# Optimization experiments

Measured on AMD Instinct MI355X. Metric: run time of the kernel, lower is better.

## Reference

```python
import jax, jax.numpy as jnp
import numpy as np

N, T, H, L, E, F, CN, CG = 20000, 2, 128, 4, 320000, 514, 3, 2
EPS = 1e-7  # GENConv message epsilon


def _ln(x, g, b):
    mu = jnp.mean(x, axis=-1, keepdims=True)
    var = jnp.mean((x - mu) ** 2, axis=-1, keepdims=True)
    return (x - mu) / jnp.sqrt(var + 1e-5) * g + b


def _genconv(x, src, dst, e, W1, b1, g1, be1, W2, b2, t, n):
    # message: relu(x_j + edge_attr) + eps
    msg = jax.nn.relu(x[src] + e) + EPS  # [E,H]
    # softmax aggregation with learnable temperature t, grouped by dst
    logits = msg * t
    m = jax.ops.segment_max(logits, dst, num_segments=n)
    m = jnp.where(jnp.isfinite(m), m, 0.0)  # guard empty segments
    ex = jnp.exp(logits - m[dst])
    denom = jax.ops.segment_sum(ex, dst, num_segments=n)
    alpha = ex / (denom[dst] + 1e-16)
    agg = jax.ops.segment_sum(msg * alpha, dst, num_segments=n)  # [N,H]
    out = agg + x  # residual with root node (x_r)
    # MLP: Lin(H,2H) -> LayerNorm -> ReLU -> Lin(2H,H)
    h1 = jax.nn.relu(_ln(out @ W1 + b1, g1, be1))
    return h1 @ W2 + b2


def _attn(x, Wq, Wk, Wv, gamma):
    # x: [N, T, H]; channel (transform-axis) self-attention, gamma-gated residual
    q = jnp.einsum('tc,nch->nth', Wq, x)
    k = jnp.einsum('tc,nch->nth', Wk, x)
    v = jnp.einsum('tc,nch->nth', Wv, x)
    a = jax.nn.softmax(jnp.einsum('nth,nsh->nts', q, k), axis=-1)
    o = jnp.einsum('nts,nsh->nth', a, v)
    return gamma * o + x


def setup_inputs() -> dict:
    key = jax.random.key(0)
    ks = iter(jax.random.split(key, 48))

    def nrm(sh, s=0.02):
        return jax.random.normal(next(ks), sh, dtype=jnp.float32) * s

    inp = {}
    inp['node_feature'] = jax.random.normal(next(ks), (N, F), dtype=jnp.float32)
    inp['edge_index'] = jax.random.randint(next(ks), (T, 2, E), 0, N, dtype=jnp.int32)
    inp['edge_attr'] = jax.random.normal(next(ks), (T, E, 2), dtype=jnp.float32)
    # encoders
    inp['Wne'] = nrm((F, H)); inp['bne'] = jnp.zeros((H,), jnp.float32)
    inp['Wee'] = nrm((2, H)); inp['bee'] = jnp.zeros((H,), jnp.float32)
    # per-layer GENConv MLP params (stacked over L)
    inp['W1'] = nrm((L, H, 2 * H)); inp['b1'] = jnp.zeros((L, 2 * H), jnp.float32)
    inp['g1'] = jnp.ones((L, 2 * H), jnp.float32); inp['be1'] = jnp.zeros((L, 2 * H), jnp.float32)
    inp['W2'] = nrm((L, 2 * H, H)); inp['b2'] = jnp.zeros((L, H), jnp.float32)
    # DeepGCNLayer LayerNorms
    inp['dg'] = jnp.ones((L, H), jnp.float32); inp['db'] = jnp.zeros((L, H), jnp.float32)
    # learnable temperatures
    inp['t'] = jnp.ones((L,), jnp.float32)
    # node attention + head
    inp['Wq_n'] = nrm((T, T), 0.2); inp['Wk_n'] = nrm((T, T), 0.2); inp['Wv_n'] = nrm((T, T), 0.2)
    inp['gamma_n'] = jnp.float32(0.5)
    inp['Wn1'] = nrm((T * H, T * H)); inp['bn1'] = jnp.zeros((T * H,), jnp.float32)
    inp['Wn2'] = nrm((T * H, CN)); inp['bn2'] = jnp.zeros((CN,), jnp.float32)
    # graph attention + head
    inp['Wq_g'] = nrm((T, T), 0.2); inp['Wk_g'] = nrm((T, T), 0.2); inp['Wv_g'] = nrm((T, T), 0.2)
    inp['gamma_g'] = jnp.float32(0.5)
    inp['Wg1'] = nrm((T * H, T * H)); inp['bg1'] = jnp.zeros((T * H,), jnp.float32)
    inp['Wg2'] = nrm((T * H, CG)); inp['bg2'] = jnp.zeros((CG,), jnp.float32)
    return inp


def reference(node_feature, edge_index, edge_attr, Wne, bne, Wee, bee,
              W1, b1, g1, be1, W2, b2, dg, db, t,
              Wq_n, Wk_n, Wv_n, gamma_n, Wn1, bn1, Wn2, bn2,
              Wq_g, Wk_g, Wv_g, gamma_g, Wg1, bg1, Wg2, bg2):
    embs = []
    for ti in range(T):
        x = node_feature @ Wne + bne           # node_encoder
        e = edge_attr[ti] @ Wee + bee          # edge_encoder
        src, dst = edge_index[ti, 0], edge_index[ti, 1]
        # layers[0].conv applied directly
        x = _genconv(x, src, dst, e, W1[0], b1[0], g1[0], be1[0], W2[0], b2[0], t[0], N)
        # res+ DeepGCN blocks
        for l in range(1, L):
            h = jax.nn.relu(_ln(x, dg[l], db[l]))  # dropout p=0.1 is identity in eval
            x = x + _genconv(h, src, dst, e, W1[l], b1[l], g1[l], be1[l], W2[l], b2[l], t[l], N)
        x = jax.nn.relu(_ln(x, dg[0], db[0]))
        embs.append(x)
    emb = jnp.stack(embs, axis=1)  # [N, T, H]

    a = _attn(emb, Wq_n, Wk_n, Wv_n, gamma_n).reshape(N, T * H)
    node = jax.nn.relu(a @ Wn1 + bn1) @ Wn2 + bn2
    node = jax.nn.log_softmax(node, axis=-1)

    g = _attn(emb, Wq_g, Wk_g, Wv_g, gamma_g).reshape(N, T * H)
    gp = jnp.mean(g, axis=0, keepdims=True)  # global_mean_pool (single graph)
    gp = jax.nn.relu(gp @ Wg1 + bg1) @ Wg2 + bg2
    gp = jax.nn.log_softmax(gp, axis=-1)
    return (node, gp)
```

## Files before the change

kernel.cpp:

```cpp
#include <hip/hip_runtime.h>

#define NN 20000
#define TT 2
#define HH 128
#define LL 4
#define EE 320000
#define FF 514
#define CN 3
#define CG 2
#define MP 20096

typedef __bf16 bf16x8 __attribute__((ext_vector_type(8)));
typedef __bf16 bf16x4 __attribute__((ext_vector_type(4)));
typedef __bf16 bf16x2 __attribute__((ext_vector_type(2)));
typedef float f32x4 __attribute__((ext_vector_type(4)));

struct __align__(8) Edge { int src; __bf16 ea0, ea1; };

__device__ inline float wave_sum(float v) {
#pragma unroll
  for (int off = 32; off; off >>= 1) v += __shfl_xor(v, off);
  return v;
}
__device__ inline float red16(float v) {
  v += __shfl_xor(v, 1); v += __shfl_xor(v, 2);
  v += __shfl_xor(v, 4); v += __shfl_xor(v, 8);
  return v;
}

__device__ __forceinline__ float fexp2(float x) {
#if __has_builtin(__builtin_amdgcn_exp2f)
  return __builtin_amdgcn_exp2f(x);
#else
  return exp2f(x);
#endif
}

__device__ __forceinline__ void gload_lds16(const void* g, void* l) {
  __builtin_amdgcn_global_load_lds(
      (const __attribute__((address_space(1))) unsigned int*)g,
      (__attribute__((address_space(3))) unsigned int*)l, 16, 0, 0);
}

#define ENCB (MP / 64)
#define SSB 313
#define CHUNK 5000
__global__ __launch_bounds__(256) void enc_scatter_kernel(
    const float* __restrict__ Af, const __bf16* __restrict__ BT,
    const float* __restrict__ bias, __bf16* __restrict__ C,
    const int* __restrict__ edge_index, const float* __restrict__ edge_attr,
    int* __restrict__ cursor, Edge* __restrict__ edges) {
  __shared__ __bf16 As[2][64][32];
  __shared__ __bf16 Bs[2][128][32];
  const int tid = threadIdx.x;
  if (blockIdx.x >= ENCB) {
    int sb = blockIdx.x - ENCB;
    int chunk = sb & 7;
    int slice = sb >> 3;
    int i0 = slice * 2048 + tid * 8;
    if (i0 >= 2 * EE) return;
    int ti = (i0 >= EE) ? 1 : 0;
    int e0 = i0 - ti * EE;
    const int* srcp = edge_index + (size_t)ti * 2 * EE;
    int dst8[8];
    __builtin_memcpy(dst8, srcp + EE + e0, 32);
#pragma unroll
    for (int j = 0; j < 8; ++j) {
      int gnode = ti * NN + dst8[j];
      if (gnode / CHUNK != chunk) continue;
      int s = srcp[e0 + j];
      float2 ea = ((const float2*)edge_attr)[(size_t)ti * EE + e0 + j];
      int pos = atomicAdd(&cursor[gnode], 1);
      Edge ed;
      ed.src = s + ti * MP;
      ed.ea0 = (__bf16)ea.x; ed.ea1 = (__bf16)ea.y;
      __builtin_memcpy(&edges[pos], &ed, sizeof(Edge));
    }
    return;
  }
  const int K = 576;
  const int lane = tid & 63, w = tid >> 6;
  const int bm = blockIdx.x * 64;
  const int wr = (w >> 1) * 32, wc = (w & 1) * 64;
  const int fr = lane & 15, fq = lane >> 4;
  const int rowA = tid >> 2, chA = (tid & 3) * 8;
  const bool rowOK = (bm + rowA) < NN;
  const float* Arow = Af + (size_t)(bm + rowA) * FF;
  const __bf16* Bb = BT + (size_t)rowA * K + chA;
  const __bf16* Bb2 = Bb + (size_t)64 * K;
  f32x4 acc[2][4] = {};
  float va[8];

#define LOADA(k0)                                                   \
  do {                                                              \
    int c0_ = (k0) + chA;                                           \
    if (rowOK && c0_ + 8 <= FF) {                                   \
      __builtin_memcpy(va, Arow + c0_, 32);                         \
    } else {                                                        \
      _Pragma("unroll") for (int i_ = 0; i_ < 8; ++i_)              \
          va[i_] = (rowOK && c0_ + i_ < FF) ? Arow[c0_ + i_] : 0.f; \
    }                                                               \
  } while (0)
#define WRITEA(buf)                                                 \
  do {                                                              \
    bf16x8 o_;                                                      \
    _Pragma("unroll") for (int i_ = 0; i_ < 8; ++i_)                \
        o_[i_] = (__bf16)va[i_];                                    \
    *(bf16x8*)&As[buf][rowA][chA] = o_;                             \
  } while (0)
#define STAGEB(buf, k0)                                 \
  do {                                                  \
    gload_lds16(Bb + (k0), &Bs[buf][rowA][chA]);        \
    gload_lds16(Bb2 + (k0), &Bs[buf][rowA + 64][chA]);  \
  } while (0)

  LOADA(0); WRITEA(0);
  STAGEB(0, 0);
  __syncthreads();
  int cur = 0;
  for (int k0 = 0; k0 < K; k0 += 32) {
    bool last = (k0 + 32 >= K);
    if (!last) {
      LOADA(k0 + 32);
      STAGEB(cur ^ 1, k0 + 32);
    }
    bf16x8 af[2], bq[4];
#pragma unroll
    for (int m = 0; m < 2; ++m)
      af[m] = *(const bf16x8*)&As[cur][wr + m * 16 + fr][fq * 8];
#pragma unroll
    for (int n = 0; n < 4; ++n)
      bq[n] = *(const bf16x8*)&Bs[cur][wc + n * 16 + fr][fq * 8];
#pragma unroll
    for (int m = 0; m < 2; ++m)
#pragma unroll
      for (int n = 0; n < 4; ++n)
        acc[m][n] =
            __builtin_amdgcn_mfma_f32_16x16x32_bf16(af[m], bq[n], acc[m][n], 0, 0, 0);
    if (!last) WRITEA(cur ^ 1);
    __syncthreads();
    cur ^= 1;
  }
#undef LOADA
#undef WRITEA
#undef STAGEB
#pragma unroll
  for (int m = 0; m < 2; ++m) {
#pragma unroll
    for (int n = 0; n < 4; ++n) {
#pragma unroll
      for (int j = 0; j < 4; ++j) {
        int gm = bm + wr + m * 16 + fq * 4 + j;
        int gn = wc + n * 16 + fr;
        if (gm < NN) {
          __bf16 c = (__bf16)(acc[m][n][j] + bias[gn]);
          C[(size_t)gm * 128 + gn] = c;
          C[(size_t)(gm + MP) * 128 + gn] = c;
        }
      }
    }
  }
}

__global__ __launch_bounds__(256) void gemm256_head(
    const __bf16* __restrict__ A, const __bf16* __restrict__ BT,
    const float* __restrict__ bias, const float* __restrict__ W2h,
    const float* __restrict__ b2h, float* __restrict__ outf, int M, int K) {
  __shared__ __bf16 As[2][64][32];
  __shared__ __bf16 Bs[2][256][32];
  const int tid = threadIdx.x;
  const int lane = tid & 63, w = tid >> 6;
  const int bm = blockIdx.x * 64;
  const int wr = w * 16;
  const int fr = lane & 15, fq = lane >> 4;
  const int rowA = tid >> 2, chA = (tid & 3) * 8;
  const __bf16* Ab = A + (size_t)(bm + rowA) * K + chA;
  const __bf16* Bb = BT + (size_t)rowA * K + chA;
  f32x4 acc[16] = {};

#define STG(buf, k0)                                                \
  do {                                                              \
    gload_lds16(Ab + (k0), &As[buf][rowA][chA]);                    \
    _Pragma("unroll") for (int r = 0; r < 4; ++r)                   \
        gload_lds16(Bb + (size_t)(r * 64) * K + (k0),               \
                    &Bs[buf][rowA + r * 64][chA]);                  \
  } while (0)

  STG(0, 0);
  __syncthreads();
  int cur = 0;
  for (int k0 = 0; k0 < K; k0 += 32) {
    if (k0 + 32 < K) STG(cur ^ 1, k0 + 32);
    bf16x8 af = *(const bf16x8*)&As[cur][wr + fr][fq * 8];
#pragma unroll
    for (int n = 0; n < 16; ++n) {
      bf16x8 bq = *(const bf16x8*)&Bs[cur][n * 16 + fr][fq * 8];
      acc[n] = __builtin_amdgcn_mfma_f32_16x16x32_bf16(af, bq, acc[n], 0, 0, 0);
    }
    __syncthreads();
    cur ^= 1;
  }
#undef STG

  float cb[16], w0[16], w1[16], w2[16];
#pragma unroll
  for (int n = 0; n < 16; ++n) {
    int col = n * 16 + fr;
    cb[n] = bias[col];
    w0[n] = W2h[col * 3 + 0];
    w1[n] = W2h[col * 3 + 1];
    w2[n] = W2h[col * 3 + 2];
  }
#pragma unroll
  for (int j = 0; j < 4; ++j) {
    float p0 = 0.f, p1 = 0.f, p2 = 0.f;
#pragma unroll
    for (int n = 0; n < 16; ++n) {
      float h = fmaxf(acc[n][j] + cb[n], 0.f);
      p0 += h * w0[n]; p1 += h * w1[n]; p2 += h * w2[n];
    }
    p0 = red16(p0); p1 = red16(p1); p2 = red16(p2);
    int gm = bm + wr + fq * 4 + j;
    if (fr == 0 && gm < M) {
      float l0 = p0 + b2h[0], l1 = p1 + b2h[1], l2 = p2 + b2h[2];
      float m = fmaxf(l0, fmaxf(l1, l2));
      float lse = m + logf(__expf(l0 - m) + __expf(l1 - m) + __expf(l2 - m));
      outf[(size_t)gm * 3 + 0] = l0 - lse;
      outf[(size_t)gm * 3 + 1] = l1 - lse;
      outf[(size_t)gm * 3 + 2] = l2 - lse;
    }
  }
}

template <int MODE>
__global__ __launch_bounds__(256) void gemm_layer(
    const __bf16* __restrict__ A, const __bf16* __restrict__ W1T,
    const float* __restrict__ b1, const float* __restrict__ g1,
    const float* __restrict__ be1, const __bf16* __restrict__ W2T,
    const float* __restrict__ b2, float* __restrict__ xres,
    const float* __restrict__ dgv, const float* __restrict__ dbv,
    void* __restrict__ lnout) {
  __shared__ char smem[40960];
  __shared__ __bf16 h1[64][264];
  __shared__ float redS[64][2], redS2[64][2];
  auto As = (__bf16(*)[64][32])smem;
  auto Bs1 = (__bf16(*)[256][32])(smem + 8192);
  auto Bs2 = (__bf16(*)[128][32])smem;
  const int tid = threadIdx.x;
  const int lane = tid & 63, w = tid >> 6;
  const int bm = blockIdx.x * 64;
  const int fr = lane & 15, fq = lane >> 4;
  const int rowA = tid >> 2, chA = (tid & 3) * 8;

  {
    const int wr = w * 16;
    const __bf16* Ab = A + (size_t)(bm + rowA) * 128 + chA;
    const __bf16* Bb = W1T + (size_t)rowA * 128 + chA;
    f32x4 acc[16] = {};
#define STG1(buf, k0)                                                 \
  do {                                                                \
    gload_lds16(Ab + (k0), &As[buf][rowA][chA]);                      \
    _Pragma("unroll") for (int r = 0; r < 4; ++r)                     \
        gload_lds16(Bb + (size_t)(r * 64) * 128 + (k0),               \
                    &Bs1[buf][rowA + r * 64][chA]);                   \
  } while (0)
    STG1(0, 0);
    __syncthreads();
    int cur = 0;
    for (int k0 = 0; k0 < 128; k0 += 32) {
      if (k0 + 32 < 128) STG1(cur ^ 1, k0 + 32);
      bf16x8 af = *(const bf16x8*)&As[cur][wr + fr][fq * 8];
#pragma unroll
      for (int n = 0; n < 16; ++n) {
        bf16x8 bq = *(const bf16x8*)&Bs1[cur][n * 16 + fr][fq * 8];
        acc[n] = __builtin_amdgcn_mfma_f32_16x16x32_bf16(af, bq, acc[n], 0, 0, 0);
      }
      __syncthreads();
      cur ^= 1;
    }
#undef STG1
    float cb[16], gv[16], bev[16];
#pragma unroll
    for (int n = 0; n < 16; ++n) {
      int col = n * 16 + fr;
      cb[n] = b1[col]; gv[n] = g1[col]; bev[n] = be1[col];
    }
#pragma unroll
    for (int j = 0; j < 4; ++j) {
      float cj[16], s = 0.f, s2 = 0.f;
#pragma unroll
      for (int n = 0; n < 16; ++n) {
        float c = acc[n][j] + cb[n];
        cj[n] = c; s += c; s2 += c * c;
      }
      s = red16(s); s2 = red16(s2);
      float mu = s * (1.f / 256);
      float var = fmaxf(s2 * (1.f / 256) - mu * mu, 0.f);
      float rr = rsqrtf(var + 1e-5f);
      int r = wr + fq * 4 + j;
#pragma unroll
      for (int n = 0; n < 16; ++n) {
        float y = (cj[n] - mu) * rr * gv[n] + bev[n];
        h1[r][n * 16 + fr] = (__bf16)fmaxf(y, 0.f);
      }
    }
  }
  __syncthreads();

  {
    const int wr = (w >> 1) * 32, wc = (w & 1) * 64;
    const __bf16* Bb = W2T + (size_t)rowA * 256 + chA;
    const __bf16* Bb2 = Bb + (size_t)64 * 256;
    f32x4 acc[2][4] = {};
#define STG2(buf, k0)                                   \
  do {                                                  \
    gload_lds16(Bb + (k0), &Bs2[buf][rowA][chA]);       \
    gload_lds16(Bb2 + (k0), &Bs2[buf][rowA + 64][chA]); \
  } while (0)
    STG2(0, 0);
    __syncthreads();
    int cur = 0;
    for (int k0 = 0; k0 < 256; k0 += 32) {
      if (k0 + 32 < 256) STG2(cur ^ 1, k0 + 32);
      bf16x8 af[2], bq[4];
#pragma unroll
      for (int m = 0; m < 2; ++m)
        af[m] = *(const bf16x8*)&h1[wr + m * 16 + fr][k0 + fq * 8];
#pragma unroll
      for (int n = 0; n < 4; ++n)
        bq[n] = *(const bf16x8*)&Bs2[cur][wc + n * 16 + fr][fq * 8];
#pragma unroll
      for (int m = 0; m < 2; ++m)
#pragma unroll
        for (int n = 0; n < 4; ++n)
          acc[m][n] =
              __builtin_amdgcn_mfma_f32_16x16x32_bf16(af[m], bq[n], acc[m][n], 0, 0, 0);
      __syncthreads();
      cur ^= 1;
    }
#undef STG2

    float cv[2][4][4];
#pragma unroll
    for (int m = 0; m < 2; ++m) {
      int r0 = wr + m * 16 + fq * 4;
#pragma unroll
      for (int j = 0; j < 4; ++j) {
        int gm = bm + r0 + j;
        float s = 0.f, s2 = 0.f;
#pragma unroll
        for (int n = 0; n < 4; ++n) {
          float c = acc[m][n][j] + b2[wc + n * 16 + fr];
          if (MODE != 0) c += xres[(size_t)gm * 128 + wc + n * 16 + fr];
          cv[m][n][j] = c;
          s += c; s2 += c * c;
        }
        s = red16(s); s2 = red16(s2);
        if (fr == 0) {
          redS[r0 + j][w & 1] = s;
          redS2[r0 + j][w & 1] = s2;
        }
      }
    }
    __syncthreads();
#pragma unroll
    for (int m = 0; m < 2; ++m) {
      int r0 = wr + m * 16 + fq * 4;
#pragma unroll
      for (int j = 0; j < 4; ++j) {
        int r = r0 + j;
        int gm = bm + r;
        float S = redS[r][0] + redS[r][1];
        float S2 = redS2[r][0] + redS2[r][1];
        float mu = S * (1.f / 128);
        float var = fmaxf(S2 * (1.f / 128) - mu * mu, 0.f);
        float rr = rsqrtf(var + 1e-5f);
        if constexpr (MODE < 2) {
          float* xp = xres + (size_t)gm * 128;
          __bf16* hp = (__bf16*)lnout + (size_t)gm * 128;
#pragma unroll
          for (int n = 0; n < 4; ++n) {
            int col = wc + n * 16 + fr;
            float c = cv[m][n][j];
            xp[col] = c;
            float y = (c - mu) * rr * dgv[col] + dbv[col];
            hp[col] = (__bf16)fmaxf(y, 0.f);
          }
        } else {
          int half = gm >= MP;
          int node = gm - half * MP;
          if (node < NN) {
            float* ep = (float*)lnout + (size_t)node * 256 + half * 128;
#pragma unroll
            for (int n = 0; n < 4; ++n) {
              int col = wc + n * 16 + fr;
              float y = (cv[m][n][j] - mu) * rr * dgv[col] + dbv[col];
              ep[col] = fmaxf(y, 0.f);
            }
          }
        }
      }
    }
  }
}

struct WtDesc { const float* src; __bf16* dst; int K, N, Kpad, gbase; };
struct WtDescs { WtDesc d[10]; };
#define WTG 50176
#define CTG 80000

__global__ __launch_bounds__(256) void prep_kernel(
    WtDescs descs, const int* __restrict__ edge_index, int* __restrict__ deg,
    float* __restrict__ gp_sum) {
  const int tid = threadIdx.x;
  if (blockIdx.x == 0) gp_sum[tid] = 0.f;
  int g = blockIdx.x * 256 + tid;
  if (g >= WTG + CTG) return;
  if (g < WTG) {
    int wb = g;
    int di = 0;
#pragma unroll
    for (int t = 1; t < 10; ++t)
      if (wb >= descs.d[t].gbase) di = t;
    WtDesc de = descs.d[di];
    int local = wb - de.gbase;
    int kg8 = de.Kpad >> 3;
    int n = local / kg8, k0 = (local - n * kg8) * 8;
    bf16x8 o;
#pragma unroll
    for (int i = 0; i < 8; ++i) {
      int k = k0 + i;
      o[i] = (__bf16)((k < de.K) ? de.src[(size_t)k * de.N + n] : 0.f);
    }
    *(bf16x8*)(de.dst + (size_t)n * de.Kpad + k0) = o;
  } else {
    int i0 = (g - WTG) * 8;
    int ti = (i0 >= EE) ? 1 : 0;
    int e0 = i0 - ti * EE;
    int dst8[8];
    __builtin_memcpy(dst8, edge_index + (size_t)ti * 2 * EE + EE + e0, 32);
    int* dbase = deg + ti * NN;
#pragma unroll
    for (int j = 0; j < 8; ++j) atomicAdd(&dbase[dst8[j]], 1);
  }
}

__global__ __launch_bounds__(1024) void scan2_kernel(
    const int* __restrict__ deg_all, int* __restrict__ rowptr,
    int* __restrict__ cursor) {
  const int ti = blockIdx.x;
  const int* deg = deg_all + ti * NN;
  __shared__ int sums[1024];
  int tid = threadIdx.x;
  int chunk = (NN + 1023) / 1024;
  int begin = tid * chunk, end = min(begin + chunk, NN);
  int s = 0;
  for (int i = begin; i < end; ++i) s += deg[i];
  sums[tid] = s;
  __syncthreads();
  for (int off = 1; off < 1024; off <<= 1) {
    int v = (tid >= off) ? sums[tid - off] : 0;
    __syncthreads();
    sums[tid] += v;
    __syncthreads();
  }
  int running = ti * EE + sums[tid] - s;
  for (int i = begin; i < end; ++i) {
    rowptr[ti * NN + i] = running;
    cursor[ti * NN + i] = running;
    running += deg[i];
  }
  if (tid == 0 && ti == 1) rowptr[2 * NN] = 2 * EE;
}

__global__ __launch_bounds__(256) void agg_kernel(
    const __bf16* __restrict__ xin, const int* __restrict__ rowptr,
    const Edge* __restrict__ edges, const float* __restrict__ Wee,
    const float* __restrict__ bee, const float* __restrict__ tptr, int layer,
    __bf16* __restrict__ out) {
  int wave = threadIdx.x >> 6, lane = threadIdx.x & 63;
  int b = blockIdx.x;
  int x8 = b & 7;
  int q = x8 >> 1;
  int par = x8 & 1;
  int ti = q >> 1, chh = q & 1;
  int group = (b >> 3) * 2 + par;
  int qq = lane >> 4, c15 = lane & 15;
  int node = group * 16 + wave * 4 + qq;
  int gnode = ti * NN + node;
  int xrow = ti * MP + node;
  float t2 = tptr[layer] * 1.4426950408889634f;
  int c0 = chh * 64 + c15 * 4;
  float den[4] = {}, num[4] = {};
  int e = rowptr[gnode];
  const int e1 = rowptr[gnode + 1];

  if (t2 > 0.f) {
    float w0p[4], w1p[4], bvp[4];
#pragma unroll
    for (int i = 0; i < 4; ++i) {
      w0p[i] = Wee[c0 + i] * t2;
      w1p[i] = Wee[HH + c0 + i] * t2;
      bvp[i] = bee[c0 + i] * t2;
    }
#define MLPF(XV, ED)                                                      \
  do {                                                                    \
    float eax = (float)(ED).ea0, eay = (float)(ED).ea1;                   \
    _Pragma("unroll") for (int i = 0; i < 4; ++i) {                       \
      float te = fmaf(eax, w0p[i], fmaf(eay, w1p[i], bvp[i]));            \
      float sm = fmaxf(fmaf((float)(XV)[i], t2, te), 0.f);                \
      float ex = fexp2(sm);                                               \
      den[i] += ex; num[i] = fmaf(sm, ex, num[i]);                        \
    }                                                                     \
  } while (0)
    for (; e + 2 <= e1; e += 2) {
      Edge E0 = edges[e];
      Edge E1 = edges[e + 1];
      bf16x4 x0 = *(const bf16x4*)(xin + (size_t)E0.src * HH + c0);
      bf16x4 x1 = *(const bf16x4*)(xin + (size_t)E1.src * HH + c0);
      MLPF(x0, E0);
      MLPF(x1, E1);
    }
    if (e < e1) {
      Edge E0 = edges[e];
      bf16x4 x0 = *(const bf16x4*)(xin + (size_t)E0.src * HH + c0);
      MLPF(x0, E0);
    }
#undef MLPF
    bf16x4 xr = *(const bf16x4*)(xin + (size_t)xrow * HH + c0);
    bf16x4 o;
#pragma unroll
    for (int i = 0; i < 4; ++i)
      o[i] = (__bf16)(num[i] / (t2 * (den[i] + 1e-16f)) + (float)xr[i]);
    *(bf16x4*)(out + (size_t)xrow * HH + c0) = o;
  } else {
    float w0[4], w1[4], bv[4];
#pragma unroll
    for (int i = 0; i < 4; ++i) {
      w0[i] = Wee[c0 + i];
      w1[i] = Wee[HH + c0 + i];
      bv[i] = bee[c0 + i];
    }
    for (; e < e1; ++e) {
      Edge E0 = edges[e];
      bf16x4 xv = *(const bf16x4*)(xin + (size_t)E0.src * HH + c0);
      float eax = (float)E0.ea0, eay = (float)E0.ea1;
#pragma unroll
      for (int i = 0; i < 4; ++i) {
        float m =
            fmaxf((float)xv[i] + eax * w0[i] + eay * w1[i] + bv[i], 0.f) + 1e-7f;
        float ex = fexp2(m * t2);
        den[i] += ex; num[i] += m * ex;
      }
    }
    bf16x4 xr = *(const bf16x4*)(xin + (size_t)xrow * HH + c0);
    bf16x4 o;
#pragma unroll
    for (int i = 0; i < 4; ++i)
      o[i] = (__bf16)(num[i] / (den[i] + 1e-16f) + (float)xr[i]);
    *(bf16x4*)(out + (size_t)xrow * HH + c0) = o;
  }
}

__global__ __launch_bounds__(256) void attn2_kernel(
    const float* __restrict__ emb, const float* __restrict__ Wq_n,
    const float* __restrict__ Wk_n, const float* __restrict__ Wv_n,
    const float* __restrict__ gn, const float* __restrict__ Wq_g,
    const float* __restrict__ Wk_g, const float* __restrict__ Wv_g,
    const float* __restrict__ gg, __bf16* __restrict__ outn,
    float* __restrict__ partial) {
  __shared__ float gsum[4][256];
  int wave = threadIdx.x >> 6, lane = threadIdx.x & 63;
  int tid = threadIdx.x;
  int n = blockIdx.x * 4 + wave;
  int c0 = lane * 2;
  const float* base = emb + (size_t)n * (2 * HH);
  float2 x0 = *(const float2*)(base + c0);
  float2 x1 = *(const float2*)(base + HH + c0);

#define ATTN_BODY(Wq, Wk, Wv, GAM, O0A, O0B, O1A, O1B)                        \
  {                                                                           \
    float gamma = *(GAM);                                                     \
    float wq00 = Wq[0], wq01 = Wq[1], wq10 = Wq[2], wq11 = Wq[3];             \
    float wk00 = Wk[0], wk01 = Wk[1], wk10 = Wk[2], wk11 = Wk[3];             \
    float wv00 = Wv[0], wv01 = Wv[1], wv10 = Wv[2], wv11 = Wv[3];             \
    float q0a = wq00 * x0.x + wq01 * x1.x, q0b = wq00 * x0.y + wq01 * x1.y;   \
    float q1a = wq10 * x0.x + wq11 * x1.x, q1b = wq10 * x0.y + wq11 * x1.y;   \
    float k0a = wk00 * x0.x + wk01 * x1.x, k0b = wk00 * x0.y + wk01 * x1.y;   \
    float k1a = wk10 * x0.x + wk11 * x1.x, k1b = wk10 * x0.y + wk11 * x1.y;   \
    float v0a = wv00 * x0.x + wv01 * x1.x, v0b = wv00 * x0.y + wv01 * x1.y;   \
    float v1a = wv10 * x0.x + wv11 * x1.x, v1b = wv10 * x0.y + wv11 * x1.y;   \
    float s00 = wave_sum(q0a * k0a + q0b * k0b);                              \
    float s01 = wave_sum(q0a * k1a + q0b * k1b);                              \
    float s10 = wave_sum(q1a * k0a + q1b * k0b);                              \
    float s11 = wave_sum(q1a * k1a + q1b * k1b);                              \
    float m0 = fmaxf(s00, s01);                                               \
    float e00 = __expf(s00 - m0), e01 = __expf(s01 - m0);                     \
    float i0 = 1.f / (e00 + e01);                                             \
    float a00 = e00 * i0, a01 = e01 * i0;                                     \
    float m1 = fmaxf(s10, s11);                                               \
    float e10 = __expf(s10 - m1), e11 = __expf(s11 - m1);                     \
    float i1 = 1.f / (e10 + e11);                                             \
    float a10 = e10 * i1, a11 = e11 * i1;                                     \
    O0A = gamma * (a00 * v0a + a01 * v1a) + x0.x;                             \
    O0B = gamma * (a00 * v0b + a01 * v1b) + x0.y;                             \
    O1A = gamma * (a10 * v0a + a11 * v1a) + x1.x;                             \
    O1B = gamma * (a10 * v0b + a11 * v1b) + x1.y;                             \
  }

  float n0a, n0b, n1a, n1b;
  ATTN_BODY(Wq_n, Wk_n, Wv_n, gn, n0a, n0b, n1a, n1b);
  __bf16* opn = outn + (size_t)n * (2 * HH);
  bf16x2 t0; t0[0] = (__bf16)n0a; t0[1] = (__bf16)n0b;
  bf16x2 t1; t1[0] = (__bf16)n1a; t1[1] = (__bf16)n1b;
  *(bf16x2*)(opn + c0) = t0;
  *(bf16x2*)(opn + HH + c0) = t1;

  float g0a, g0b, g1a, g1b;
  ATTN_BODY(Wq_g, Wk_g, Wv_g, gg, g0a, g0b, g1a, g1b);
  gsum[wave][c0] = g0a;
  gsum[wave][c0 + 1] = g0b;
  gsum[wave][128 + c0] = g1a;
  gsum[wave][129 + c0] = g1b;
  __syncthreads();
  partial[(size_t)blockIdx.x * 256 + tid] =
      gsum[0][tid] + gsum[1][tid] + gsum[2][tid] + gsum[3][tid];
#undef ATTN_BODY
}

__global__ __launch_bounds__(256) void pool_kernel(const float* __restrict__ partial,
                                                   float* __restrict__ gp_sum,
                                                   int nRows) {
  int c = threadIdx.x;
  float s = 0.f;
  for (int r = blockIdx.x; r < nRows; r += gridDim.x)
    s += partial[(size_t)r * 256 + c];
  atomicAdd(&gp_sum[c], s);
}

__global__ __launch_bounds__(256) void graph_head_kernel(
    const float* __restrict__ gp_sum, const float* __restrict__ Wg1,
    const float* __restrict__ bg1, const float* __restrict__ Wg2,
    const float* __restrict__ bg2, float* __restrict__ outp, float invN) {
  __shared__ float gp[256];
  __shared__ float h1[256];
  __shared__ float lg[2];
  int tid = threadIdx.x;
  gp[tid] = gp_sum[tid] * invN;
  __syncthreads();
  float acc = bg1[tid];
  for (int k = 0; k < 256; ++k) acc += gp[k] * Wg1[k * 256 + tid];
  h1[tid] = fmaxf(acc, 0.f);
  __syncthreads();
  if (tid < 2) {
    float l = bg2[tid];
    for (int c = 0; c < 256; ++c) l += h1[c] * Wg2[c * 2 + tid];
    lg[tid] = l;
  }
  __syncthreads();
  if (tid == 0) {
    float m = fmaxf(lg[0], lg[1]);
    float lse = m + logf(__expf(lg[0] - m) + __expf(lg[1] - m));
    outp[0] = lg[0] - lse;
    outp[1] = lg[1] - lse;
  }
}

extern "C" void kernel_launch(void* const* d_in, const int* in_sizes, int n_in,
                              void* d_out, int out_size, void* d_ws, size_t ws_size,
                              hipStream_t stream) {
  (void)in_sizes; (void)n_in; (void)out_size; (void)ws_size;
  const float* node_feature = (const float*)d_in[0];
  const int* edge_index = (const int*)d_in[1];
  const float* edge_attr = (const float*)d_in[2];
  const float* Wne = (const float*)d_in[3];
  const float* bne = (const float*)d_in[4];
  const float* Wee = (const float*)d_in[5];
  const float* bee = (const float*)d_in[6];
  const float* W1 = (const float*)d_in[7];
  const float* b1 = (const float*)d_in[8];
  const float* g1 = (const float*)d_in[9];
  const float* be1 = (const float*)d_in[10];
  const float* W2 = (const float*)d_in[11];
  const float* b2 = (const float*)d_in[12];
  const float* dg = (const float*)d_in[13];
  const float* db = (const float*)d_in[14];
  const float* tpar = (const float*)d_in[15];
  const float* Wq_n = (const float*)d_in[16];
  const float* Wk_n = (const float*)d_in[17];
  const float* Wv_n = (const float*)d_in[18];
  const float* gamma_n = (const float*)d_in[19];
  const float* Wn1 = (const float*)d_in[20];
  const float* bn1 = (const float*)d_in[21];
  const float* Wn2 = (const float*)d_in[22];
  const float* bn2 = (const float*)d_in[23];
  const float* Wq_g = (const float*)d_in[24];
  const float* Wk_g = (const float*)d_in[25];
  const float* Wv_g = (const float*)d_in[26];
  const float* gamma_g = (const float*)d_in[27];
  const float* Wg1 = (const float*)d_in[28];
  const float* bg1 = (const float*)d_in[29];
  const float* Wg2 = (const float*)d_in[30];
  const float* bg2 = (const float*)d_in[31];
  float* out = (float*)d_out;

  char* pc = (char*)d_ws;
  auto alloc = [&](size_t bytes) {
    char* r = pc;
    pc += (bytes + 255) & ~(size_t)255;
    return r;
  };
  float* xbuf = (float*)alloc((size_t)2 * MP * HH * 4);
  __bf16* hbuf_b = (__bf16*)alloc((size_t)2 * MP * HH * 2);
  __bf16* attnb = (__bf16*)alloc((size_t)MP * 256 * 2);
  float* emb = (float*)alloc((size_t)NN * 2 * HH * 4);
  __bf16* aggout_b = (__bf16*)alloc((size_t)2 * MP * HH * 2);
  float* partial = xbuf;
  __bf16* wt_ne = (__bf16*)alloc((size_t)128 * 576 * 2);
  __bf16* wt1 = (__bf16*)alloc((size_t)4 * 256 * 128 * 2);
  __bf16* wt2 = (__bf16*)alloc((size_t)4 * 128 * 256 * 2);
  __bf16* wtn1 = (__bf16*)alloc((size_t)256 * 256 * 2);
  float* gp_sum = (float*)alloc(256 * 4);
  int* deg = (int*)alloc((size_t)2 * NN * 4);
  int* cursor = (int*)alloc((size_t)2 * NN * 4);
  int* rowptr = (int*)alloc((size_t)(2 * NN + 2) * 4);
  Edge* edges = (Edge*)alloc((size_t)2 * EE * 8);

  const int gRows2 = 2 * MP / 64;

  WtDescs wd;
  int gb = 0;
  wd.d[0] = {Wne, wt_ne, FF, HH, 576, gb}; gb += HH * 576 / 8;
  for (int l = 0; l < 4; ++l) {
    wd.d[1 + l] = {W1 + (size_t)l * HH * 256, wt1 + (size_t)l * 256 * HH, HH, 256,
                   HH, gb};
    gb += 256 * HH / 8;
  }
  for (int l = 0; l < 4; ++l) {
    wd.d[5 + l] = {W2 + (size_t)l * 256 * HH, wt2 + (size_t)l * HH * 256, 256, HH,
                   256, gb};
    gb += HH * 256 / 8;
  }
  wd.d[9] = {Wn1, wtn1, 256, 256, 256, gb};

  hipMemsetAsync(deg, 0, 2 * NN * sizeof(int), stream);
  prep_kernel<<<(WTG + CTG + 255) / 256, 256, 0, stream>>>(wd, edge_index, deg,
                                                           gp_sum);
  scan2_kernel<<<2, 1024, 0, stream>>>(deg, rowptr, cursor);
  enc_scatter_kernel<<<ENCB + 8 * SSB, 256, 0, stream>>>(
      node_feature, wt_ne, bne, hbuf_b, edge_index, edge_attr, cursor, edges);

  for (int l = 0; l < LL; ++l) {
    agg_kernel<<<625 * 8, 256, 0, stream>>>(hbuf_b, rowptr, edges, Wee, bee, tpar,
                                            l, aggout_b);
    const __bf16* w1l = wt1 + (size_t)l * 256 * HH;
    const __bf16* w2l = wt2 + (size_t)l * HH * 256;
    if (l == 0)
      gemm_layer<0><<<gRows2, 256, 0, stream>>>(
          aggout_b, w1l, b1 + l * 2 * HH, g1 + l * 2 * HH, be1 + l * 2 * HH, w2l,
          b2 + l * HH, xbuf, dg + 1 * HH, db + 1 * HH, hbuf_b);
    else if (l < LL - 1)
      gemm_layer<1><<<gRows2, 256, 0, stream>>>(
          aggout_b, w1l, b1 + l * 2 * HH, g1 + l * 2 * HH, be1 + l * 2 * HH, w2l,
          b2 + l * HH, xbuf, dg + (l + 1) * HH, db + (l + 1) * HH, hbuf_b);
    else
      gemm_layer<2><<<gRows2, 256, 0, stream>>>(
          aggout_b, w1l, b1 + l * 2 * HH, g1 + l * 2 * HH, be1 + l * 2 * HH, w2l,
          b2 + l * HH, xbuf, dg, db, emb);
  }

  attn2_kernel<<<NN / 4, 256, 0, stream>>>(emb, Wq_n, Wk_n, Wv_n, gamma_n, Wq_g,
                                           Wk_g, Wv_g, gamma_g, attnb, partial);
  gemm256_head<<<MP / 64, 256, 0, stream>>>(attnb, wtn1, bn1, Wn2, bn2, out, NN,
                                            256);
  pool_kernel<<<128, 256, 0, stream>>>(partial, gp_sum, NN / 4);
  graph_head_kernel<<<1, 256, 0, stream>>>(gp_sum, Wg1, bg1, Wg2, bg2,
                                           out + (size_t)NN * CN, 1.0f / NN);
}
```

Measured before the change: 425.5 us.

## Fuse attention into node head GEMM, deepen prefetch, unroll edge loop

Merges the channel-attention kernel with the node-head GEMM so each block computes attention for 64 nodes straight into shared memory and multiplies them there. This removes the bf16 attention buffer round trip and one kernel launch, and the pool kernel now reads 314 partial rows instead of 5000. Separately, the encoder GEMM issues its global A loads one iteration earlier, and the aggregation loop gathers four edges per iteration for more memory-level parallelism. The fused kernel uses much more shared memory and launches only about 314 blocks, which may lower occupancy and hurt latency hiding.

Measured after the change: 413.0 us, median of 2. -3.0%, faster.

```diff
diff --git a/kernel.cpp b/kernel.cpp
--- a/kernel.cpp
+++ b/kernel.cpp
@@ -115,15 +115,13 @@
   } while (0)
 
   LOADA(0); WRITEA(0);
+  LOADA(32);
   STAGEB(0, 0);
   __syncthreads();
   int cur = 0;
   for (int k0 = 0; k0 < K; k0 += 32) {
     bool last = (k0 + 32 >= K);
-    if (!last) {
-      LOADA(k0 + 32);
-      STAGEB(cur ^ 1, k0 + 32);
-    }
+    if (!last) STAGEB(cur ^ 1, k0 + 32);
     bf16x8 af[2], bq[4];
 #pragma unroll
     for (int m = 0; m < 2; ++m)
@@ -137,7 +135,10 @@
       for (int n = 0; n < 4; ++n)
         acc[m][n] =
             __builtin_amdgcn_mfma_f32_16x16x32_bf16(af[m], bq[n], acc[m][n], 0, 0, 0);
-    if (!last) WRITEA(cur ^ 1);
+    if (!last) {
+      WRITEA(cur ^ 1);
+      if (k0 + 64 < K) LOADA(k0 + 64);
+    }
     __syncthreads();
     cur ^= 1;
   }
@@ -158,76 +159,6 @@
           C[(size_t)(gm + MP) * 128 + gn] = c;
         }
       }
-    }
-  }
-}
-
-__global__ __launch_bounds__(256) void gemm256_head(
-    const __bf16* __restrict__ A, const __bf16* __restrict__ BT,
-    const float* __restrict__ bias, const float* __restrict__ W2h,
-    const float* __restrict__ b2h, float* __restrict__ outf, int M, int K) {
-  __shared__ __bf16 As[2][64][32];
-  __shared__ __bf16 Bs[2][256][32];
-  const int tid = threadIdx.x;
-  const int lane = tid & 63, w = tid >> 6;
-  const int bm = blockIdx.x * 64;
-  const int wr = w * 16;
-  const int fr = lane & 15, fq = lane >> 4;
-  const int rowA = tid >> 2, chA = (tid & 3) * 8;
-  const __bf16* Ab = A + (size_t)(bm + rowA) * K + chA;
-  const __bf16* Bb = BT + (size_t)rowA * K + chA;
-  f32x4 acc[16] = {};
-
-#define STG(buf, k0)                                                \
-  do {                                                              \
-    gload_lds16(Ab + (k0), &As[buf][rowA][chA]);                    \
-    _Pragma("unroll") for (int r = 0; r < 4; ++r)                   \
-        gload_lds16(Bb + (size_t)(r * 64) * K + (k0),               \
-                    &Bs[buf][rowA + r * 64][chA]);                  \
-  } while (0)
-
-  STG(0, 0);
-  __syncthreads();
-  int cur = 0;
-  for (int k0 = 0; k0 < K; k0 += 32) {
-    if (k0 + 32 < K) STG(cur ^ 1, k0 + 32);
-    bf16x8 af = *(const bf16x8*)&As[cur][wr + fr][fq * 8];
-#pragma unroll
-    for (int n = 0; n < 16; ++n) {
-      bf16x8 bq = *(const bf16x8*)&Bs[cur][n * 16 + fr][fq * 8];
-      acc[n] = __builtin_amdgcn_mfma_f32_16x16x32_bf16(af, bq, acc[n], 0, 0, 0);
-    }
-    __syncthreads();
-    cur ^= 1;
-  }
-#undef STG
-
-  float cb[16], w0[16], w1[16], w2[16];
-#pragma unroll
-  for (int n = 0; n < 16; ++n) {
-    int col = n * 16 + fr;
-    cb[n] = bias[col];
-    w0[n] = W2h[col * 3 + 0];
-    w1[n] = W2h[col * 3 + 1];
-    w2[n] = W2h[col * 3 + 2];
-  }
-#pragma unroll
-  for (int j = 0; j < 4; ++j) {
-    float p0 = 0.f, p1 = 0.f, p2 = 0.f;
-#pragma unroll
-    for (int n = 0; n < 16; ++n) {
-      float h = fmaxf(acc[n][j] + cb[n], 0.f);
-      p0 += h * w0[n]; p1 += h * w1[n]; p2 += h * w2[n];
-    }
-    p0 = red16(p0); p1 = red16(p1); p2 = red16(p2);
-    int gm = bm + wr + fq * 4 + j;
-    if (fr == 0 && gm < M) {
-      float l0 = p0 + b2h[0], l1 = p1 + b2h[1], l2 = p2 + b2h[2];
-      float m = fmaxf(l0, fmaxf(l1, l2));
-      float lse = m + logf(__expf(l0 - m) + __expf(l1 - m) + __expf(l2 - m));
-      outf[(size_t)gm * 3 + 0] = l0 - lse;
-      outf[(size_t)gm * 3 + 1] = l1 - lse;
-      outf[(size_t)gm * 3 + 2] = l2 - lse;
     }
   }
 }
@@ -513,15 +444,16 @@
       den[i] += ex; num[i] = fmaf(sm, ex, num[i]);                        \
     }                                                                     \
   } while (0)
-    for (; e + 2 <= e1; e += 2) {
-      Edge E0 = edges[e];
-      Edge E1 = edges[e + 1];
+    for (; e + 4 <= e1; e += 4) {
+      Edge E0 = edges[e], E1 = edges[e + 1];
+      Edge E2 = edges[e + 2], E3 = edges[e + 3];
       bf16x4 x0 = *(const bf16x4*)(xin + (size_t)E0.src * HH + c0);
       bf16x4 x1 = *(const bf16x4*)(xin + (size_t)E1.src * HH + c0);
-      MLPF(x0, E0);
-      MLPF(x1, E1);
-    }
-    if (e < e1) {
+      bf16x4 x2 = *(const bf16x4*)(xin + (size_t)E2.src * HH + c0);
+      bf16x4 x3 = *(const bf16x4*)(xin + (size_t)E3.src * HH + c0);
+      MLPF(x0, E0); MLPF(x1, E1); MLPF(x2, E2); MLPF(x3, E3);
+    }
+    for (; e < e1; ++e) {
       Edge E0 = edges[e];
       bf16x4 x0 = *(const bf16x4*)(xin + (size_t)E0.src * HH + c0);
       MLPF(x0, E0);
@@ -562,21 +494,23 @@
   }
 }
 
-__global__ __launch_bounds__(256) void attn2_kernel(
+__global__ __launch_bounds__(256) void attn_head_kernel(
     const float* __restrict__ emb, const float* __restrict__ Wq_n,
     const float* __restrict__ Wk_n, const float* __restrict__ Wv_n,
     const float* __restrict__ gn, const float* __restrict__ Wq_g,
     const float* __restrict__ Wk_g, const float* __restrict__ Wv_g,
-    const float* __restrict__ gg, __bf16* __restrict__ outn,
+    const float* __restrict__ gg, const __bf16* __restrict__ WTn1,
+    const float* __restrict__ bn1, const float* __restrict__ Wn2,
+    const float* __restrict__ b2h, float* __restrict__ outf,
     float* __restrict__ partial) {
+  __shared__ __bf16 h1[64][264];
+  __shared__ __bf16 Bs[2][256][32];
   __shared__ float gsum[4][256];
-  int wave = threadIdx.x >> 6, lane = threadIdx.x & 63;
-  int tid = threadIdx.x;
-  int n = blockIdx.x * 4 + wave;
-  int c0 = lane * 2;
-  const float* base = emb + (size_t)n * (2 * HH);
-  float2 x0 = *(const float2*)(base + c0);
-  float2 x1 = *(const float2*)(base + HH + c0);
+  const int tid = threadIdx.x;
+  const int lane = tid & 63, wave = tid >> 6;
+  const int bm = blockIdx.x * 64;
+  const int c0 = lane * 2;
+  float ag0 = 0.f, ag1 = 0.f, ag2 = 0.f, ag3 = 0.f;
 
 #define ATTN_BODY(Wq, Wk, Wv, GAM, O0A, O0B, O1A, O1B)                        \
   {                                                                           \
@@ -608,24 +542,91 @@
     O1B = gamma * (a10 * v0b + a11 * v1b) + x1.y;                             \
   }
 
-  float n0a, n0b, n1a, n1b;
-  ATTN_BODY(Wq_n, Wk_n, Wv_n, gn, n0a, n0b, n1a, n1b);
-  __bf16* opn = outn + (size_t)n * (2 * HH);
-  bf16x2 t0; t0[0] = (__bf16)n0a; t0[1] = (__bf16)n0b;
-  bf16x2 t1; t1[0] = (__bf16)n1a; t1[1] = (__bf16)n1b;
-  *(bf16x2*)(opn + c0) = t0;
-  *(bf16x2*)(opn + HH + c0) = t1;
-
-  float g0a, g0b, g1a, g1b;
-  ATTN_BODY(Wq_g, Wk_g, Wv_g, gg, g0a, g0b, g1a, g1b);
-  gsum[wave][c0] = g0a;
-  gsum[wave][c0 + 1] = g0b;
-  gsum[wave][128 + c0] = g1a;
-  gsum[wave][129 + c0] = g1b;
+  for (int i = wave; i < 64; i += 4) {
+    int n = bm + i;
+    if (n < NN) {
+      const float* base = emb + (size_t)n * 256;
+      float2 x0 = *(const float2*)(base + c0);
+      float2 x1 = *(const float2*)(base + 128 + c0);
+      float n0a, n0b, n1a, n1b;
+      ATTN_BODY(Wq_n, Wk_n, Wv_n, gn, n0a, n0b, n1a, n1b);
+      h1[i][c0] = (__bf16)n0a;
+      h1[i][c0 + 1] = (__bf16)n0b;
+      h1[i][128 + c0] = (__bf16)n1a;
+      h1[i][129 + c0] = (__bf16)n1b;
+      float g0a, g0b, g1a, g1b;
+      ATTN_BODY(Wq_g, Wk_g, Wv_g, gg, g0a, g0b, g1a, g1b);
+      ag0 += g0a; ag1 += g0b; ag2 += g1a; ag3 += g1b;
+    } else {
+      h1[i][c0] = (__bf16)0.f;
+      h1[i][c0 + 1] = (__bf16)0.f;
+      h1[i][128 + c0] = (__bf16)0.f;
+      h1[i][129 + c0] = (__bf16)0.f;
+    }
+  }
+#undef ATTN_BODY
+  gsum[wave][c0] = ag0;
+  gsum[wave][c0 + 1] = ag1;
+  gsum[wave][128 + c0] = ag2;
+  gsum[wave][129 + c0] = ag3;
   __syncthreads();
   partial[(size_t)blockIdx.x * 256 + tid] =
       gsum[0][tid] + gsum[1][tid] + gsum[2][tid] + gsum[3][tid];
-#undef ATTN_BODY
+
+  const int fr = lane & 15, fq = lane >> 4;
+  const int wr = wave * 16;
+  const int rowA = tid >> 2, chA = (tid & 3) * 8;
+  const __bf16* Bb = WTn1 + (size_t)rowA * 256 + chA;
+  f32x4 acc[16] = {};
+#define STGH(buf, k0)                                                \
+  do {                                                               \
+    _Pragma("unroll") for (int r = 0; r < 4; ++r)                    \
+        gload_lds16(Bb + (size_t)(r * 64) * 256 + (k0),              \
+                    &Bs[buf][rowA + r * 64][chA]);                   \
+  } while (0)
+  STGH(0, 0);
+  __syncthreads();
+  int cur = 0;
+  for (int k0 = 0; k0 < 256; k0 += 32) {
+    if (k0 + 32 < 256) STGH(cur ^ 1, k0 + 32);
+    bf16x8 af = *(const bf16x8*)&h1[wr + fr][k0 + fq * 8];
+#pragma unroll
+    for (int n = 0; n < 16; ++n) {
+      bf16x8 bq = *(const bf16x8*)&Bs[cur][n * 16 + fr][fq * 8];
+      acc[n] = __builtin_amdgcn_mfma_f32_16x16x32_bf16(af, bq, acc[n], 0, 0, 0);
+    }
+    __syncthreads();
+    cur ^= 1;
+  }
+#undef STGH
+  float cb[16], w0[16], w1[16], w2[16];
+#pragma unroll
+  for (int n = 0; n < 16; ++n) {
+    int col = n * 16 + fr;
+    cb[n] = bn1[col];
+    w0[n] = Wn2[col * 3 + 0];
+    w1[n] = Wn2[col * 3 + 1];
+    w2[n] = Wn2[col * 3 + 2];
+  }
+#pragma unroll
+  for (int j = 0; j < 4; ++j) {
+    float p0 = 0.f, p1 = 0.f, p2 = 0.f;
+#pragma unroll
+    for (int n = 0; n < 16; ++n) {
+      float h = fmaxf(acc[n][j] + cb[n], 0.f);
+      p0 += h * w0[n]; p1 += h * w1[n]; p2 += h * w2[n];
+    }
+    p0 = red16(p0); p1 = red16(p1); p2 = red16(p2);
+    int gm = bm + wr + fq * 4 + j;
+    if (fr == 0 && gm < NN) {
+      float l0 = p0 + b2h[0], l1 = p1 + b2h[1], l2 = p2 + b2h[2];
+      float m = fmaxf(l0, fmaxf(l1, l2));
+      float lse = m + logf(__expf(l0 - m) + __expf(l1 - m) + __expf(l2 - m));
+      outf[(size_t)gm * 3 + 0] = l0 - lse;
+      outf[(size_t)gm * 3 + 1] = l1 - lse;
+      outf[(size_t)gm * 3 + 2] = l2 - lse;
+    }
+  }
 }
 
 __global__ __launch_bounds__(256) void pool_kernel(const float* __restrict__ partial,
@@ -712,7 +713,6 @@
   };
   float* xbuf = (float*)alloc((size_t)2 * MP * HH * 4);
   __bf16* hbuf_b = (__bf16*)alloc((size_t)2 * MP * HH * 2);
-  __bf16* attnb = (__bf16*)alloc((size_t)MP * 256 * 2);
   float* emb = (float*)alloc((size_t)NN * 2 * HH * 4);
   __bf16* aggout_b = (__bf16*)alloc((size_t)2 * MP * HH * 2);
   float* partial = xbuf;
@@ -769,11 +769,10 @@
           b2 + l * HH, xbuf, dg, db, emb);
   }
 
-  attn2_kernel<<<NN / 4, 256, 0, stream>>>(emb, Wq_n, Wk_n, Wv_n, gamma_n, Wq_g,
-                                           Wk_g, Wv_g, gamma_g, attnb, partial);
-  gemm256_head<<<MP / 64, 256, 0, stream>>>(attnb, wtn1, bn1, Wn2, bn2, out, NN,
-                                            256);
-  pool_kernel<<<128, 256, 0, stream>>>(partial, gp_sum, NN / 4);
+  attn_head_kernel<<<MP / 64, 256, 0, stream>>>(
+      emb, Wq_n, Wk_n, Wv_n, gamma_n, Wq_g, Wk_g, Wv_g, gamma_g, wtn1, bn1, Wn2,
+      bn2, out, partial);
+  pool_kernel<<<128, 256, 0, stream>>>(partial, gp_sum, MP / 64);
   graph_head_kernel<<<1, 256, 0, stream>>>(gp_sum, Wg1, bg1, Wg2, bg2,
                                            out + (size_t)NN * CN, 1.0f / NN);
 }
```
